# Kernel tuning notes

Hardware: AMD Instinct MI355X
Metric: run time of the kernel (lower is better)

Reference implementation:

```python
import jax, jax.numpy as jnp
import numpy as np

NUM_SEGMENTS = 440  # ~ 256*256/150 superpixels as in the original SLIC call
C_FEAT = 2112       # hypercolumn channel sum hard-coded in nn.Linear(2112, 1024)
H = W = 256
D = 32


def setup_inputs() -> dict:
    key = jax.random.key(0)
    ks = jax.random.split(key, 12)
    inp = {
        "feature_maps": jax.random.normal(ks[0], (C_FEAT, H, W), dtype=jnp.float32),
        "sp": jax.random.randint(ks[1], (H, W), 0, NUM_SEGMENTS, dtype=jnp.int32),
        "y": jax.random.randint(ks[2], (H, W), 0, 3, dtype=jnp.int32),
        "W1": jax.random.normal(ks[3], (C_FEAT, 1024), dtype=jnp.float32) * 0.02,
        "b1": jax.random.normal(ks[4], (1024,), dtype=jnp.float32) * 0.02,
        "W2": jax.random.normal(ks[5], (1024, 1024), dtype=jnp.float32) * 0.02,
        "b2": jax.random.normal(ks[6], (1024,), dtype=jnp.float32) * 0.02,
        "W3": jax.random.normal(ks[7], (1024, D), dtype=jnp.float32) * 0.02,
        "b3": jax.random.normal(ks[8], (D,), dtype=jnp.float32) * 0.02,
        "Wc": jax.random.normal(ks[9], (D, 2), dtype=jnp.float32) * 0.02,
        "bc": jax.random.normal(ks[10], (2,), dtype=jnp.float32) * 0.02,
    }
    return inp


def reference(feature_maps, sp, y, W1, b1, W2, b2, W3, b3, Wc, bc):
    S = NUM_SEGMENTS
    C = feature_maps.shape[0]
    fm = feature_maps.reshape(C, -1).T          # [HW, C] pixel hypercolumns
    seg = sp.reshape(-1)                        # [HW] superpixel ids

    # --- superpixel mean-pool (segment reduce; torch did per-segment nonzero+mean) ---
    sums = jax.ops.segment_sum(fm, seg, num_segments=S)                      # [S, C]
    counts = jax.ops.segment_sum(jnp.ones_like(seg, dtype=fm.dtype), seg,
                                 num_segments=S)                             # [S]
    feat = sums / jnp.maximum(counts, 1.0)[:, None]                          # [S, C]

    # --- per-segment MLP + softmax classifier ---
    h = jax.nn.relu(feat @ W1 + b1)
    h = jax.nn.relu(h @ W2 + b2)
    h = jax.nn.relu(h @ W3 + b3)
    pred = jax.nn.softmax(h @ Wc + bc, axis=-1)                              # [S, 2]

    # --- majority label per segment with the original tie rule ---
    onehot = jax.nn.one_hot(y.reshape(-1), 3, dtype=jnp.float32)             # [HW, 3]
    hist = jax.ops.segment_sum(onehot, seg, num_segments=S)                  # [S, 3]
    lab = jnp.argmax(hist, axis=1).astype(jnp.int32)
    ones_c, twos_c = hist[:, 1], hist[:, 2]
    lab = jnp.where(lab == 0,
                    jnp.where(twos_c > ones_c, 2,
                              jnp.where(ones_c > twos_c, 1, 0)).astype(jnp.int32),
                    lab)

    # --- label propagation: aff[i,j] = exp(-cos(feat_i, feat_j)), propagate from
    #     labeled (lab!=0) to unlabeled (lab==0) when max affinity >= 0.7 ---
    feat_d = jax.lax.stop_gradient(feat)        # original detaches feat here
    fn = feat_d / jnp.linalg.norm(feat_d, axis=1, keepdims=True)
    aff = jnp.exp(-(fn @ fn.T))                 # [S, S]
    labeled = lab != 0
    aff_m = jnp.where(labeled[None, :], aff, -jnp.inf)
    maX = jnp.max(aff_m, axis=1)
    mIdx = jnp.argmax(aff_m, axis=1)
    new_lab = jnp.where((lab == 0) & (maX >= 0.7), lab[mIdx], lab)
    return pred, new_lab
```

## Files before the change

kernel.cpp:

```cpp
#include <hip/hip_runtime.h>
#include <math.h>

#define NSEG 440
#define CF   2112
#define HW   65536
#define NH   1024

#define OFF_HIST 0
#define OFF_FEAT 2048
#define OFF_H1   931328
#define OFF_H2   1381888
#define OFF_AFF  1832448
#define OFF_INVN 2026048
#define OFF_LAB  2026488

__global__ __launch_bounds__(256) void hist_kernel(const int* __restrict__ sp,
                                                   const int* __restrict__ y,
                                                   float* __restrict__ hist) {
    __shared__ float lh[NSEG * 3];
    int t = threadIdx.x;
    for (int i = t; i < NSEG * 3; i += 256) lh[i] = 0.0f;
    __syncthreads();
    int idx = blockIdx.x * 256 + t;
    for (int p = idx; p < HW; p += 64 * 256) {
        int s  = sp[p];
        int yy = y[p];
        atomicAdd(&lh[s * 3 + yy], 1.0f);
    }
    __syncthreads();
    for (int i = t; i < NSEG * 3; i += 256)
        if (lh[i] != 0.0f) atomicAdd(&hist[i], lh[i]);
}

__global__ __launch_bounds__(256) void segsum_kernel(const float* __restrict__ fm,
                                                     const int* __restrict__ sp,
                                                     const float* __restrict__ hist,
                                                     float* __restrict__ feat) {
    __shared__ float seg[NSEG];
    int t = threadIdx.x;
    int c = blockIdx.x;
    for (int s = t; s < NSEG; s += 256) seg[s] = 0.0f;
    __syncthreads();
    const float* f = fm + (size_t)c * HW;
    for (int it = 0; it < 64; ++it) {
        int p = it * 1024 + t * 4;
        float4 v = *(const float4*)(f + p);
        int4  si = *(const int4*)(sp + p);
        atomicAdd(&seg[si.x], v.x);
        atomicAdd(&seg[si.y], v.y);
        atomicAdd(&seg[si.z], v.z);
        atomicAdd(&seg[si.w], v.w);
    }
    __syncthreads();
    for (int s = t; s < NSEG; s += 256) {
        float cnt = hist[3 * s] + hist[3 * s + 1] + hist[3 * s + 2];
        feat[(size_t)s * CF + c] = seg[s] / fmaxf(cnt, 1.0f);
    }
}

__global__ void lab_kernel(const float* __restrict__ hist, int* __restrict__ lab) {
    int s = blockIdx.x * 256 + threadIdx.x;
    if (s >= NSEG) return;
    float h0 = hist[3 * s], h1 = hist[3 * s + 1], h2 = hist[3 * s + 2];
    int l = 0; float b = h0;
    if (h1 > b) { l = 1; b = h1; }
    if (h2 > b) { l = 2; b = h2; }
    if (l == 0) l = (h2 > h1) ? 2 : ((h1 > h2) ? 1 : 0);
    lab[s] = l;
}

template <int RELU>
__global__ __launch_bounds__(256) void gemm_nn(const float* __restrict__ A,
                                               const float* __restrict__ B,
                                               const float* __restrict__ bias,
                                               float* __restrict__ C,
                                               int M, int N, int K) {
    __shared__ __align__(16) float As[16][64];
    __shared__ __align__(16) float Bs[16][64];
    int t  = threadIdx.x;
    int n0 = blockIdx.x * 64;
    int m0 = blockIdx.y * 64;
    int ty = t >> 4, tx = t & 15;
    int arow = t >> 2, acol = (t & 3) * 4;
    int brow = t >> 4, bcol = (t & 15) * 4;
    float acc[4][4] = {};
    for (int k0 = 0; k0 < K; k0 += 16) {
        float4 av;
        int m = m0 + arow;
        if (m < M) av = *(const float4*)(A + (size_t)m * K + k0 + acol);
        else       av = make_float4(0.f, 0.f, 0.f, 0.f);
        As[acol + 0][arow] = av.x;
        As[acol + 1][arow] = av.y;
        As[acol + 2][arow] = av.z;
        As[acol + 3][arow] = av.w;
        float4 bv = *(const float4*)(B + (size_t)(k0 + brow) * N + n0 + bcol);
        *(float4*)&Bs[brow][bcol] = bv;
        __syncthreads();
#pragma unroll
        for (int kk = 0; kk < 16; ++kk) {
            float4 a = *(const float4*)&As[kk][ty * 4];
            float4 b = *(const float4*)&Bs[kk][tx * 4];
            float ar[4] = {a.x, a.y, a.z, a.w};
            float br[4] = {b.x, b.y, b.z, b.w};
#pragma unroll
            for (int i = 0; i < 4; ++i)
#pragma unroll
                for (int j = 0; j < 4; ++j) acc[i][j] += ar[i] * br[j];
        }
        __syncthreads();
    }
#pragma unroll
    for (int i = 0; i < 4; ++i) {
        int m = m0 + ty * 4 + i;
        if (m < M) {
#pragma unroll
            for (int j = 0; j < 4; ++j) {
                int n = n0 + tx * 4 + j;
                float v = acc[i][j] + bias[n];
                if (RELU) v = fmaxf(v, 0.0f);
                C[(size_t)m * N + n] = v;
            }
        }
    }
}

__global__ __launch_bounds__(256) void norm_kernel(const float* __restrict__ feat,
                                                   float* __restrict__ invn) {
    int s = blockIdx.x;
    int t = threadIdx.x;
    const float* r = feat + (size_t)s * CF;
    float acc = 0.0f;
    for (int c = t * 4; c < CF; c += 1024) {
        float4 v = *(const float4*)(r + c);
        acc += v.x * v.x + v.y * v.y + v.z * v.z + v.w * v.w;
    }
    for (int off = 32; off; off >>= 1) acc += __shfl_down(acc, off);
    __shared__ float w[4];
    if ((t & 63) == 0) w[t >> 6] = acc;
    __syncthreads();
    if (t == 0) {
        float tot = w[0] + w[1] + w[2] + w[3];
        invn[s] = 1.0f / sqrtf(fmaxf(tot, 1e-30f));
    }
}

__global__ __launch_bounds__(256) void gemm_nt_aff(const float* __restrict__ feat,
                                                   const float* __restrict__ invn,
                                                   float* __restrict__ aff) {
    __shared__ __align__(16) float As[16][64];
    __shared__ __align__(16) float Bs[16][64];
    int t  = threadIdx.x;
    int n0 = blockIdx.x * 64;
    int m0 = blockIdx.y * 64;
    int ty = t >> 4, tx = t & 15;
    int arow = t >> 2, acol = (t & 3) * 4;
    float acc[4][4] = {};
    for (int k0 = 0; k0 < CF; k0 += 16) {
        float4 av, bv;
        int m = m0 + arow;
        if (m < NSEG) av = *(const float4*)(feat + (size_t)m * CF + k0 + acol);
        else          av = make_float4(0.f, 0.f, 0.f, 0.f);
        int n = n0 + arow;
        if (n < NSEG) bv = *(const float4*)(feat + (size_t)n * CF + k0 + acol);
        else          bv = make_float4(0.f, 0.f, 0.f, 0.f);
        As[acol + 0][arow] = av.x;
        As[acol + 1][arow] = av.y;
        As[acol + 2][arow] = av.z;
        As[acol + 3][arow] = av.w;
        Bs[acol + 0][arow] = bv.x;
        Bs[acol + 1][arow] = bv.y;
        Bs[acol + 2][arow] = bv.z;
        Bs[acol + 3][arow] = bv.w;
        __syncthreads();
#pragma unroll
        for (int kk = 0; kk < 16; ++kk) {
            float4 a = *(const float4*)&As[kk][ty * 4];
            float4 b = *(const float4*)&Bs[kk][tx * 4];
            float ar[4] = {a.x, a.y, a.z, a.w};
            float br[4] = {b.x, b.y, b.z, b.w};
#pragma unroll
            for (int i = 0; i < 4; ++i)
#pragma unroll
                for (int j = 0; j < 4; ++j) acc[i][j] += ar[i] * br[j];
        }
        __syncthreads();
    }
#pragma unroll
    for (int i = 0; i < 4; ++i) {
        int m = m0 + ty * 4 + i;
        if (m < NSEG) {
            float im = invn[m];
#pragma unroll
            for (int j = 0; j < 4; ++j) {
                int n = n0 + tx * 4 + j;
                if (n < NSEG)
                    aff[(size_t)m * NSEG + n] = expf(-acc[i][j] * im * invn[n]);
            }
        }
    }
}

__global__ __launch_bounds__(256) void head_kernel(const float* __restrict__ h2,
                                                   const float* __restrict__ W3,
                                                   const float* __restrict__ b3,
                                                   const float* __restrict__ Wc,
                                                   const float* __restrict__ bc,
                                                   float* __restrict__ out) {
    int s = blockIdx.x;
    int t = threadIdx.x;
    int d = t & 31, p = t >> 5;
    const float* row = h2 + (size_t)s * NH;
    float acc = 0.0f;
    int kend = p * 128 + 128;
    for (int k = p * 128; k < kend; ++k) acc += row[k] * W3[k * 32 + d];
    __shared__ float red[8][32];
    __shared__ float h3[32];
    red[p][d] = acc;
    __syncthreads();
    if (t < 32) {
        float v = 0.0f;
#pragma unroll
        for (int q = 0; q < 8; ++q) v += red[q][t];
        v += b3[t];
        h3[t] = fmaxf(v, 0.0f);
    }
    __syncthreads();
    if (t == 0) {
        float l0 = bc[0], l1 = bc[1];
#pragma unroll
        for (int dd = 0; dd < 32; ++dd) {
            l0 += h3[dd] * Wc[2 * dd];
            l1 += h3[dd] * Wc[2 * dd + 1];
        }
        float m  = fmaxf(l0, l1);
        float e0 = expf(l0 - m), e1 = expf(l1 - m);
        float inv = 1.0f / (e0 + e1);
        out[2 * s]     = e0 * inv;
        out[2 * s + 1] = e1 * inv;
    }
}

__global__ void newlab_kernel(const float* __restrict__ aff,
                              const int* __restrict__ lab,
                              float* __restrict__ out) {
    int i    = blockIdx.x;
    int lane = threadIdx.x;
    float best = -INFINITY;
    int   bidx = 0x7FFFFFFF;
    for (int j = lane; j < NSEG; j += 64) {
        if (lab[j] != 0) {
            float v = aff[(size_t)i * NSEG + j];
            if (v > best) { best = v; bidx = j; }
        }
    }
    for (int off = 32; off; off >>= 1) {
        float ov = __shfl_down(best, off);
        int   oi = __shfl_down(bidx, off);
        if (ov > best || (ov == best && oi < bidx)) { best = ov; bidx = oi; }
    }
    if (lane == 0) {
        int li = lab[i];
        int nl = li;
        if (li == 0 && best >= 0.7f && bidx != 0x7FFFFFFF) nl = lab[bidx];
        out[880 + i] = (float)nl;
    }
}

extern "C" void kernel_launch(void* const* d_in, const int* in_sizes, int n_in,
                              void* d_out, int out_size, void* d_ws, size_t ws_size,
                              hipStream_t stream) {
    const float* fm = (const float*)d_in[0];
    const int*   sp = (const int*)d_in[1];
    const int*   y  = (const int*)d_in[2];
    const float* W1 = (const float*)d_in[3];
    const float* b1 = (const float*)d_in[4];
    const float* W2 = (const float*)d_in[5];
    const float* b2 = (const float*)d_in[6];
    const float* W3 = (const float*)d_in[7];
    const float* b3 = (const float*)d_in[8];
    const float* Wc = (const float*)d_in[9];
    const float* bc = (const float*)d_in[10];
    float* out = (float*)d_out;
    float* ws  = (float*)d_ws;

    float* hist = ws + OFF_HIST;
    float* feat = ws + OFF_FEAT;
    float* h1   = ws + OFF_H1;
    float* h2   = ws + OFF_H2;
    float* aff  = ws + OFF_AFF;
    float* invn = ws + OFF_INVN;
    int*   lab  = (int*)(ws + OFF_LAB);

    hipMemsetAsync(hist, 0, NSEG * 3 * sizeof(float), stream);
    hist_kernel<<<64, 256, 0, stream>>>(sp, y, hist);
    segsum_kernel<<<CF, 256, 0, stream>>>(fm, sp, hist, feat);
    lab_kernel<<<2, 256, 0, stream>>>(hist, lab);

    gemm_nn<1><<<dim3(16, 7), 256, 0, stream>>>(feat, W1, b1, h1, NSEG, NH, CF);
    gemm_nn<1><<<dim3(16, 7), 256, 0, stream>>>(h1, W2, b2, h2, NSEG, NH, NH);
    head_kernel<<<NSEG, 256, 0, stream>>>(h2, W3, b3, Wc, bc, out);

    norm_kernel<<<NSEG, 256, 0, stream>>>(feat, invn);
    gemm_nt_aff<<<dim3(7, 7), 256, 0, stream>>>(feat, invn, aff);
    newlab_kernel<<<NSEG, 64, 0, stream>>>(aff, lab, out);
}
```

Before: 1.676 ms.

## Split-K atomic GEMMs with 128x128 tiles, move exp into newlab, batch segsum loads

The MLP and affinity GEMMs now use 128x128 tiles with 8x8 per-thread accumulators and split K across blockIdx.z, accumulating partial sums with global atomics into zeroed buffers. Bias and ReLU become separate elementwise kernels, and the exp and normalisation of the affinity move into the argmax kernel. The segment-sum loop batches eight vector loads before issuing its LDS atomics, and the histogram kernel uses vector loads across fewer blocks. The aim is more parallelism on the small-M GEMMs, which previously launched only 112 or 49 blocks. The cost is atomic contention, extra memsets and kernel launches, and non-deterministic float summation order.

```diff
diff --git a/kernel.cpp b/kernel.cpp
--- a/kernel.cpp
+++ b/kernel.cpp
@@ -6,13 +6,16 @@
 #define HW   65536
 #define NH   1024
 
+typedef float f32x4 __attribute__((ext_vector_type(4)));
+typedef int   i32x4 __attribute__((ext_vector_type(4)));
+
 #define OFF_HIST 0
-#define OFF_FEAT 2048
-#define OFF_H1   931328
-#define OFF_H2   1381888
-#define OFF_AFF  1832448
-#define OFF_INVN 2026048
-#define OFF_LAB  2026488
+#define OFF_DOT  1344
+#define OFF_INVN 194944
+#define OFF_LAB  195392
+#define OFF_FEAT 195840
+#define OFF_H1   1125120
+#define OFF_H2   1575680
 
 __global__ __launch_bounds__(256) void hist_kernel(const int* __restrict__ sp,
                                                    const int* __restrict__ y,
@@ -21,15 +24,22 @@
     int t = threadIdx.x;
     for (int i = t; i < NSEG * 3; i += 256) lh[i] = 0.0f;
     __syncthreads();
-    int idx = blockIdx.x * 256 + t;
-    for (int p = idx; p < HW; p += 64 * 256) {
-        int s  = sp[p];
-        int yy = y[p];
-        atomicAdd(&lh[s * 3 + yy], 1.0f);
-    }
-    __syncthreads();
-    for (int i = t; i < NSEG * 3; i += 256)
-        if (lh[i] != 0.0f) atomicAdd(&hist[i], lh[i]);
+    int tid = blockIdx.x * 256 + t;
+#pragma unroll
+    for (int k = 0; k < 4; ++k) {
+        int chunk = tid + k * 4096;
+        i32x4 s4 = *(const i32x4*)(sp + (size_t)chunk * 4);
+        i32x4 y4 = *(const i32x4*)(y  + (size_t)chunk * 4);
+        atomicAdd(&lh[s4.x * 3 + y4.x], 1.0f);
+        atomicAdd(&lh[s4.y * 3 + y4.y], 1.0f);
+        atomicAdd(&lh[s4.z * 3 + y4.z], 1.0f);
+        atomicAdd(&lh[s4.w * 3 + y4.w], 1.0f);
+    }
+    __syncthreads();
+    for (int i = t; i < NSEG * 3; i += 256) {
+        float v = lh[i];
+        if (v != 0.0f) atomicAdd(&hist[i], v);
+    }
 }
 
 __global__ __launch_bounds__(256) void segsum_kernel(const float* __restrict__ fm,
@@ -42,14 +52,23 @@
     for (int s = t; s < NSEG; s += 256) seg[s] = 0.0f;
     __syncthreads();
     const float* f = fm + (size_t)c * HW;
-    for (int it = 0; it < 64; ++it) {
-        int p = it * 1024 + t * 4;
-        float4 v = *(const float4*)(f + p);
-        int4  si = *(const int4*)(sp + p);
-        atomicAdd(&seg[si.x], v.x);
-        atomicAdd(&seg[si.y], v.y);
-        atomicAdd(&seg[si.z], v.z);
-        atomicAdd(&seg[si.w], v.w);
+#pragma unroll 1
+    for (int it = 0; it < 8; ++it) {
+        f32x4 v[8];
+        i32x4 q[8];
+#pragma unroll
+        for (int u = 0; u < 8; ++u) {
+            int p = (it * 8 + u) * 1024 + t * 4;
+            v[u] = *(const f32x4*)(f + p);
+            q[u] = *(const i32x4*)(sp + p);
+        }
+#pragma unroll
+        for (int u = 0; u < 8; ++u) {
+            atomicAdd(&seg[q[u].x], v[u].x);
+            atomicAdd(&seg[q[u].y], v[u].y);
+            atomicAdd(&seg[q[u].z], v[u].z);
+            atomicAdd(&seg[q[u].w], v[u].w);
+        }
     }
     __syncthreads();
     for (int s = t; s < NSEG; s += 256) {
@@ -69,59 +88,130 @@
     lab[s] = l;
 }
 
-template <int RELU>
-__global__ __launch_bounds__(256) void gemm_nn(const float* __restrict__ A,
-                                               const float* __restrict__ B,
-                                               const float* __restrict__ bias,
-                                               float* __restrict__ C,
-                                               int M, int N, int K) {
-    __shared__ __align__(16) float As[16][64];
-    __shared__ __align__(16) float Bs[16][64];
+__global__ __launch_bounds__(256) void gemm_nn_atomic(const float* __restrict__ A,
+                                                      const float* __restrict__ B,
+                                                      float* __restrict__ C,
+                                                      int M, int N, int K, int kslice) {
+    __shared__ __align__(16) float As[16][128];
+    __shared__ __align__(16) float Bs[16][128];
     int t  = threadIdx.x;
-    int n0 = blockIdx.x * 64;
-    int m0 = blockIdx.y * 64;
-    int ty = t >> 4, tx = t & 15;
-    int arow = t >> 2, acol = (t & 3) * 4;
-    int brow = t >> 4, bcol = (t & 15) * 4;
-    float acc[4][4] = {};
-    for (int k0 = 0; k0 < K; k0 += 16) {
-        float4 av;
-        int m = m0 + arow;
-        if (m < M) av = *(const float4*)(A + (size_t)m * K + k0 + acol);
-        else       av = make_float4(0.f, 0.f, 0.f, 0.f);
-        As[acol + 0][arow] = av.x;
-        As[acol + 1][arow] = av.y;
-        As[acol + 2][arow] = av.z;
-        As[acol + 3][arow] = av.w;
-        float4 bv = *(const float4*)(B + (size_t)(k0 + brow) * N + n0 + bcol);
-        *(float4*)&Bs[brow][bcol] = bv;
+    int n0 = blockIdx.x * 128;
+    int m0 = blockIdx.y * 128;
+    int kbeg = blockIdx.z * kslice;
+    int kend = kbeg + kslice;
+    int tx = t & 15, ty = t >> 4;
+    float acc[8][8] = {};
+    for (int k0 = kbeg; k0 < kend; k0 += 16) {
+#pragma unroll
+        for (int i = 0; i < 2; ++i) {
+            int slot = t * 2 + i;
+            int row = slot >> 2, c4 = (slot & 3) * 4;
+            int gm = m0 + row;
+            f32x4 v = (gm < M) ? *(const f32x4*)(A + (size_t)gm * K + k0 + c4)
+                               : (f32x4)(0.0f);
+            As[c4 + 0][row] = v.x;
+            As[c4 + 1][row] = v.y;
+            As[c4 + 2][row] = v.z;
+            As[c4 + 3][row] = v.w;
+        }
+#pragma unroll
+        for (int i = 0; i < 2; ++i) {
+            int slot = t * 2 + i;
+            int kk = slot >> 5, c4 = (slot & 31) * 4;
+            f32x4 v = *(const f32x4*)(B + (size_t)(k0 + kk) * N + n0 + c4);
+            *(f32x4*)&Bs[kk][c4] = v;
+        }
         __syncthreads();
 #pragma unroll
         for (int kk = 0; kk < 16; ++kk) {
-            float4 a = *(const float4*)&As[kk][ty * 4];
-            float4 b = *(const float4*)&Bs[kk][tx * 4];
-            float ar[4] = {a.x, a.y, a.z, a.w};
-            float br[4] = {b.x, b.y, b.z, b.w};
-#pragma unroll
-            for (int i = 0; i < 4; ++i)
-#pragma unroll
-                for (int j = 0; j < 4; ++j) acc[i][j] += ar[i] * br[j];
+            float a[8], b[8];
+            *(f32x4*)&a[0] = *(const f32x4*)&As[kk][ty * 8];
+            *(f32x4*)&a[4] = *(const f32x4*)&As[kk][ty * 8 + 4];
+            *(f32x4*)&b[0] = *(const f32x4*)&Bs[kk][tx * 8];
+            *(f32x4*)&b[4] = *(const f32x4*)&Bs[kk][tx * 8 + 4];
+#pragma unroll
+            for (int i = 0; i < 8; ++i)
+#pragma unroll
+                for (int j = 0; j < 8; ++j) acc[i][j] += a[i] * b[j];
         }
         __syncthreads();
     }
 #pragma unroll
-    for (int i = 0; i < 4; ++i) {
-        int m = m0 + ty * 4 + i;
+    for (int i = 0; i < 8; ++i) {
+        int m = m0 + ty * 8 + i;
         if (m < M) {
 #pragma unroll
-            for (int j = 0; j < 4; ++j) {
-                int n = n0 + tx * 4 + j;
-                float v = acc[i][j] + bias[n];
-                if (RELU) v = fmaxf(v, 0.0f);
-                C[(size_t)m * N + n] = v;
+            for (int j = 0; j < 8; ++j)
+                atomicAdd(&C[(size_t)m * N + n0 + tx * 8 + j], acc[i][j]);
+        }
+    }
+}
+
+__global__ __launch_bounds__(256) void gemm_nt_atomic(const float* __restrict__ A,
+                                                      float* __restrict__ C,
+                                                      int M, int K, int kslice) {
+    __shared__ __align__(16) float As[16][128];
+    __shared__ __align__(16) float Bs[16][128];
+    int t  = threadIdx.x;
+    int n0 = blockIdx.x * 128;
+    int m0 = blockIdx.y * 128;
+    int kbeg = blockIdx.z * kslice;
+    int kend = kbeg + kslice;
+    int tx = t & 15, ty = t >> 4;
+    float acc[8][8] = {};
+    for (int k0 = kbeg; k0 < kend; k0 += 16) {
+#pragma unroll
+        for (int i = 0; i < 2; ++i) {
+            int slot = t * 2 + i;
+            int row = slot >> 2, c4 = (slot & 3) * 4;
+            int gm = m0 + row;
+            f32x4 v = (gm < M) ? *(const f32x4*)(A + (size_t)gm * K + k0 + c4)
+                               : (f32x4)(0.0f);
+            As[c4 + 0][row] = v.x;
+            As[c4 + 1][row] = v.y;
+            As[c4 + 2][row] = v.z;
+            As[c4 + 3][row] = v.w;
+            int gn = n0 + row;
+            f32x4 w = (gn < M) ? *(const f32x4*)(A + (size_t)gn * K + k0 + c4)
+                               : (f32x4)(0.0f);
+            Bs[c4 + 0][row] = w.x;
+            Bs[c4 + 1][row] = w.y;
+            Bs[c4 + 2][row] = w.z;
+            Bs[c4 + 3][row] = w.w;
+        }
+        __syncthreads();
+#pragma unroll
+        for (int kk = 0; kk < 16; ++kk) {
+            float a[8], b[8];
+            *(f32x4*)&a[0] = *(const f32x4*)&As[kk][ty * 8];
+            *(f32x4*)&a[4] = *(const f32x4*)&As[kk][ty * 8 + 4];
+            *(f32x4*)&b[0] = *(const f32x4*)&Bs[kk][tx * 8];
+            *(f32x4*)&b[4] = *(const f32x4*)&Bs[kk][tx * 8 + 4];
+#pragma unroll
+            for (int i = 0; i < 8; ++i)
+#pragma unroll
+                for (int j = 0; j < 8; ++j) acc[i][j] += a[i] * b[j];
+        }
+        __syncthreads();
+    }
+#pragma unroll
+    for (int i = 0; i < 8; ++i) {
+        int m = m0 + ty * 8 + i;
+        if (m < M) {
+#pragma unroll
+            for (int j = 0; j < 8; ++j) {
+                int n = n0 + tx * 8 + j;
+                if (n < M) atomicAdd(&C[(size_t)m * M + n], acc[i][j]);
             }
         }
     }
+}
+
+__global__ __launch_bounds__(256) void bias_relu_kernel(float* __restrict__ C,
+                                                        const float* __restrict__ bias,
+                                                        int MN) {
+    int i = blockIdx.x * 256 + threadIdx.x;
+    if (i < MN) C[i] = fmaxf(C[i] + bias[i & (NH - 1)], 0.0f);
 }
 
 __global__ __launch_bounds__(256) void norm_kernel(const float* __restrict__ feat,
@@ -131,7 +221,7 @@
     const float* r = feat + (size_t)s * CF;
     float acc = 0.0f;
     for (int c = t * 4; c < CF; c += 1024) {
-        float4 v = *(const float4*)(r + c);
+        f32x4 v = *(const f32x4*)(r + c);
         acc += v.x * v.x + v.y * v.y + v.z * v.z + v.w * v.w;
     }
     for (int off = 32; off; off >>= 1) acc += __shfl_down(acc, off);
@@ -141,62 +231,6 @@
     if (t == 0) {
         float tot = w[0] + w[1] + w[2] + w[3];
         invn[s] = 1.0f / sqrtf(fmaxf(tot, 1e-30f));
-    }
-}
-
-__global__ __launch_bounds__(256) void gemm_nt_aff(const float* __restrict__ feat,
-                                                   const float* __restrict__ invn,
-                                                   float* __restrict__ aff) {
-    __shared__ __align__(16) float As[16][64];
-    __shared__ __align__(16) float Bs[16][64];
-    int t  = threadIdx.x;
-    int n0 = blockIdx.x * 64;
-    int m0 = blockIdx.y * 64;
-    int ty = t >> 4, tx = t & 15;
-    int arow = t >> 2, acol = (t & 3) * 4;
-    float acc[4][4] = {};
-    for (int k0 = 0; k0 < CF; k0 += 16) {
-        float4 av, bv;
-        int m = m0 + arow;
-        if (m < NSEG) av = *(const float4*)(feat + (size_t)m * CF + k0 + acol);
-        else          av = make_float4(0.f, 0.f, 0.f, 0.f);
-        int n = n0 + arow;
-        if (n < NSEG) bv = *(const float4*)(feat + (size_t)n * CF + k0 + acol);
-        else          bv = make_float4(0.f, 0.f, 0.f, 0.f);
-        As[acol + 0][arow] = av.x;
-        As[acol + 1][arow] = av.y;
-        As[acol + 2][arow] = av.z;
-        As[acol + 3][arow] = av.w;
-        Bs[acol + 0][arow] = bv.x;
-        Bs[acol + 1][arow] = bv.y;
-        Bs[acol + 2][arow] = bv.z;
-        Bs[acol + 3][arow] = bv.w;
-        __syncthreads();
-#pragma unroll
-        for (int kk = 0; kk < 16; ++kk) {
-            float4 a = *(const float4*)&As[kk][ty * 4];
-            float4 b = *(const float4*)&Bs[kk][tx * 4];
-            float ar[4] = {a.x, a.y, a.z, a.w};
-            float br[4] = {b.x, b.y, b.z, b.w};
-#pragma unroll
-            for (int i = 0; i < 4; ++i)
-#pragma unroll
-                for (int j = 0; j < 4; ++j) acc[i][j] += ar[i] * br[j];
-        }
-        __syncthreads();
-    }
-#pragma unroll
-    for (int i = 0; i < 4; ++i) {
-        int m = m0 + ty * 4 + i;
-        if (m < NSEG) {
-            float im = invn[m];
-#pragma unroll
-            for (int j = 0; j < 4; ++j) {
-                int n = n0 + tx * 4 + j;
-                if (n < NSEG)
-                    aff[(size_t)m * NSEG + n] = expf(-acc[i][j] * im * invn[n]);
-            }
-        }
     }
 }
 
@@ -240,16 +274,18 @@
     }
 }
 
-__global__ void newlab_kernel(const float* __restrict__ aff,
+__global__ void newlab_kernel(const float* __restrict__ dot,
+                              const float* __restrict__ invn,
                               const int* __restrict__ lab,
                               float* __restrict__ out) {
     int i    = blockIdx.x;
     int lane = threadIdx.x;
+    float im = invn[i];
     float best = -INFINITY;
     int   bidx = 0x7FFFFFFF;
     for (int j = lane; j < NSEG; j += 64) {
         if (lab[j] != 0) {
-            float v = aff[(size_t)i * NSEG + j];
+            float v = expf(-dot[(size_t)i * NSEG + j] * im * invn[j]);
             if (v > best) { best = v; bidx = j; }
         }
     }
@@ -284,23 +320,27 @@
     float* ws  = (float*)d_ws;
 
     float* hist = ws + OFF_HIST;
+    float* dot  = ws + OFF_DOT;
+    float* invn = ws + OFF_INVN;
+    int*   lab  = (int*)(ws + OFF_LAB);
     float* feat = ws + OFF_FEAT;
     float* h1   = ws + OFF_H1;
     float* h2   = ws + OFF_H2;
-    float* aff  = ws + OFF_AFF;
-    float* invn = ws + OFF_INVN;
-    int*   lab  = (int*)(ws + OFF_LAB);
-
-    hipMemsetAsync(hist, 0, NSEG * 3 * sizeof(float), stream);
-    hist_kernel<<<64, 256, 0, stream>>>(sp, y, hist);
+
+    hipMemsetAsync(hist, 0, (size_t)(OFF_INVN - OFF_HIST) * 4, stream);
+    hipMemsetAsync(h1, 0, (size_t)(450560 * 2) * 4, stream);
+
+    hist_kernel<<<16, 256, 0, stream>>>(sp, y, hist);
     segsum_kernel<<<CF, 256, 0, stream>>>(fm, sp, hist, feat);
     lab_kernel<<<2, 256, 0, stream>>>(hist, lab);
-
-    gemm_nn<1><<<dim3(16, 7), 256, 0, stream>>>(feat, W1, b1, h1, NSEG, NH, CF);
-    gemm_nn<1><<<dim3(16, 7), 256, 0, stream>>>(h1, W2, b2, h2, NSEG, NH, NH);
+    norm_kernel<<<NSEG, 256, 0, stream>>>(feat, invn);
+
+    gemm_nn_atomic<<<dim3(8, 4, 6), 256, 0, stream>>>(feat, W1, h1, NSEG, NH, CF, 352);
+    bias_relu_kernel<<<1760, 256, 0, stream>>>(h1, b1, NSEG * NH);
+    gemm_nn_atomic<<<dim3(8, 4, 4), 256, 0, stream>>>(h1, W2, h2, NSEG, NH, NH, 256);
+    bias_relu_kernel<<<1760, 256, 0, stream>>>(h2, b2, NSEG * NH);
     head_kernel<<<NSEG, 256, 0, stream>>>(h2, W3, b3, Wc, bc, out);
 
-    norm_kernel<<<NSEG, 256, 0, stream>>>(feat, invn);
-    gemm_nt_aff<<<dim3(7, 7), 256, 0, stream>>>(feat, invn, aff);
-    newlab_kernel<<<NSEG, 64, 0, stream>>>(aff, lab, out);
-}
+    gemm_nt_atomic<<<dim3(4, 4, 6), 256, 0, stream>>>(feat, dot, NSEG, CF, 352);
+    newlab_kernel<<<NSEG, 64, 0, stream>>>(dot, invn, lab, out);
+}
```

After: 1.717 ms. +2.4%, slower.
